# Kernel tuning notes

Measured on AMD Instinct MI355X. Metric: run time of the kernel, lower is better.

Reference implementation:

```python
import jax, jax.numpy as jnp
import numpy as np

H = 1024      # hidden_size
V = 50257     # output_size (vocab)
L = 10        # max_length

def setup_inputs() -> dict:
    key = jax.random.key(0)
    ks = jax.random.split(key, 16)
    s = 0.02
    f = jnp.float32
    return {
        "input_idx": jax.random.randint(ks[0], (1,), 0, V),
        "hidden": jax.random.normal(ks[1], (1, 1, H), f),
        "encoder_output": jax.random.normal(ks[2], (1, H), f),      # unused by forward (as in source)
        "encoder_outputs": jax.random.normal(ks[3], (L, H), f),
        "emb": jax.random.normal(ks[4], (V, H), f) * s,
        "attn_W": jax.random.normal(ks[5], (L, 2 * H), f) * s,
        "attn_b": jnp.zeros((L,), f),
        "comb_W": jax.random.normal(ks[6], (H, 2 * H), f) * s,
        "comb_b": jnp.zeros((H,), f),
        "W_ih": jax.random.normal(ks[7], (3 * H, H), f) * s,
        "W_hh": jax.random.normal(ks[8], (3 * H, H), f) * s,
        "b_ih": jnp.zeros((3 * H,), f),
        "b_hh": jnp.zeros((3 * H,), f),
        "out_W": jax.random.normal(ks[9], (V, H), f) * s,
        "out_b": jnp.zeros((V,), f),
    }

def reference(input_idx, hidden, encoder_output, encoder_outputs,
              emb, attn_W, attn_b, comb_W, comb_b,
              W_ih, W_hh, b_ih, b_hh, out_W, out_b):
    # embedding lookup, dropout = identity (eval mode)
    embedded = emb[input_idx]                       # [1, H]
    h0 = hidden[0]                                  # [1, H]
    # additive attention over encoder outputs
    concat = jnp.concatenate([embedded, h0], axis=1)            # [1, 2H]
    attn_weights = jax.nn.softmax(concat @ attn_W.T + attn_b, axis=1)  # [1, L]
    attn_applied = attn_weights @ encoder_outputs               # [1, H]
    # combine + relu
    x = jnp.concatenate([embedded, attn_applied], axis=1) @ comb_W.T + comb_b  # [1, H]
    x = jax.nn.relu(x)
    # single GRU step (torch gate order: r, z, n)
    gi = x @ W_ih.T + b_ih                          # [1, 3H]
    gh = h0 @ W_hh.T + b_hh                         # [1, 3H]
    ir, iz, in_ = jnp.split(gi, 3, axis=1)
    hr, hz, hn = jnp.split(gh, 3, axis=1)
    r = jax.nn.sigmoid(ir + hr)
    z = jax.nn.sigmoid(iz + hz)
    n = jnp.tanh(in_ + r * hn)
    h_new = (1.0 - z) * n + z * h0                  # [1, H]
    # output projection + log-softmax
    output = jax.nn.log_softmax(h_new @ out_W.T + out_b, axis=1)  # [1, V]
    return output, h_new[None], attn_weights
```

## Files before the change

### kernel.cpp

```cpp
#include <hip/hip_runtime.h>
#include <hip/hip_bf16.h>
#include <math.h>

#define H 1024
#define V 50257
#define L 10

#define RPC 16
#define NCHUNK ((V + RPC - 1) / RPC)

#define WS_AW     0
#define WS_GH     16
#define WS_HALF1  3104
#define WS_M2T    4128
#define WS_HNEW   14368
#define WS_LOGITS 15392
#define WS_PAIRS  65664

__device__ __forceinline__ float wave_reduce(float a) {
    #pragma unroll
    for (int off = 32; off > 0; off >>= 1) a += __shfl_down(a, off);
    return a;
}

__device__ __forceinline__ void lse_merge(float& m, float& s, float pm, float ps) {
    if (pm == -INFINITY) return;
    if (m == -INFINITY)  { m = pm; s = ps; }
    else if (pm <= m)    { s += ps * expf(pm - m); }
    else                 { s = s * expf(m - pm) + ps; m = pm; }
}

__device__ __forceinline__ float dot4(float4 a, float4 x) {
    return a.x * x.x + a.y * x.y + a.z * x.z + a.w * x.w;
}

__global__ __launch_bounds__(256) void k_stage1(
    const int* __restrict__ idx, const float* __restrict__ hidden,
    const float* __restrict__ enc_outs, const float* __restrict__ emb,
    const float* __restrict__ attn_W, const float* __restrict__ attn_b,
    const float* __restrict__ W_hh, const float* __restrict__ b_hh,
    const float* __restrict__ comb_W,
    float* __restrict__ ws, float* __restrict__ aw_out)
{
    const int b = blockIdx.x, t = threadIdx.x;
    const int wave = t >> 6, lane = t & 63;
    const float* erow = emb + (size_t)idx[0] * H;

    if (b == 0) {
        __shared__ float s_w[16];
        const float4* e4 = (const float4*)erow;
        const float4* h4 = (const float4*)hidden;
        for (int l = wave; l < L; l += 4) {
            const float4* w4 = (const float4*)(attn_W + (size_t)l * 2 * H);
            float acc = 0.f;
            #pragma unroll
            for (int ii = 0; ii < 8; ++ii) {
                const int i = lane + 64 * ii;
                const float4 a = w4[i];
                const float4 x = (i < 256) ? e4[i] : h4[i - 256];
                acc += dot4(a, x);
            }
            acc = wave_reduce(acc);
            if (lane == 0) s_w[l] = acc + attn_b[l];
        }
        __syncthreads();
        if (t == 0) {
            float m = -1e30f;
            #pragma unroll
            for (int l = 0; l < L; ++l) m = fmaxf(m, s_w[l]);
            float s = 0.f;
            #pragma unroll
            for (int l = 0; l < L; ++l) { s_w[l] = expf(s_w[l] - m); s += s_w[l]; }
            const float inv = 1.f / s;
            #pragma unroll
            for (int l = 0; l < L; ++l) s_w[l] *= inv;
        }
        __syncthreads();
        if (t < L) { ws[WS_AW + t] = s_w[t]; aw_out[t] = s_w[t]; }
    } else if (b <= 192) {
        const int r0 = (b - 1) * 16 + wave * 4;
        const float4* v4 = (const float4*)hidden;
        float4 hx[4];
        #pragma unroll
        for (int j = 0; j < 4; ++j) hx[j] = v4[lane + 64 * j];
        float a0 = 0.f, a1 = 0.f, a2 = 0.f, a3 = 0.f;
        const float4* w0 = (const float4*)(W_hh + (size_t)(r0 + 0) * H);
        const float4* w1 = (const float4*)(W_hh + (size_t)(r0 + 1) * H);
        const float4* w2 = (const float4*)(W_hh + (size_t)(r0 + 2) * H);
        const float4* w3 = (const float4*)(W_hh + (size_t)(r0 + 3) * H);
        #pragma unroll
        for (int j = 0; j < 4; ++j) {
            const int i = lane + 64 * j;
            a0 += dot4(w0[i], hx[j]); a1 += dot4(w1[i], hx[j]);
            a2 += dot4(w2[i], hx[j]); a3 += dot4(w3[i], hx[j]);
        }
        a0 = wave_reduce(a0); a1 = wave_reduce(a1);
        a2 = wave_reduce(a2); a3 = wave_reduce(a3);
        if (lane == 0) {
            ws[WS_GH + r0 + 0] = a0 + b_hh[r0 + 0];
            ws[WS_GH + r0 + 1] = a1 + b_hh[r0 + 1];
            ws[WS_GH + r0 + 2] = a2 + b_hh[r0 + 2];
            ws[WS_GH + r0 + 3] = a3 + b_hh[r0 + 3];
        }
    } else if (b <= 256) {
        const int r0 = (b - 193) * 16 + wave * 4;
        const float4* e4 = (const float4*)erow;
        float4 ex[4];
        #pragma unroll
        for (int j = 0; j < 4; ++j) ex[j] = e4[lane + 64 * j];
        float a0 = 0.f, a1 = 0.f, a2 = 0.f, a3 = 0.f;
        const float4* w0 = (const float4*)(comb_W + (size_t)(r0 + 0) * 2 * H);
        const float4* w1 = (const float4*)(comb_W + (size_t)(r0 + 1) * 2 * H);
        const float4* w2 = (const float4*)(comb_W + (size_t)(r0 + 2) * 2 * H);
        const float4* w3 = (const float4*)(comb_W + (size_t)(r0 + 3) * 2 * H);
        #pragma unroll
        for (int j = 0; j < 4; ++j) {
            const int i = lane + 64 * j;
            a0 += dot4(w0[i], ex[j]); a1 += dot4(w1[i], ex[j]);
            a2 += dot4(w2[i], ex[j]); a3 += dot4(w3[i], ex[j]);
        }
        a0 = wave_reduce(a0); a1 = wave_reduce(a1);
        a2 = wave_reduce(a2); a3 = wave_reduce(a3);
        if (lane == 0) {
            ws[WS_HALF1 + r0 + 0] = a0; ws[WS_HALF1 + r0 + 1] = a1;
            ws[WS_HALF1 + r0 + 2] = a2; ws[WS_HALF1 + r0 + 3] = a3;
        }
    } else {
        const int r = (b - 257) * 4 + wave;
        const float4* w4 = (const float4*)(comb_W + (size_t)r * 2 * H + H);
        float acc[L];
        #pragma unroll
        for (int l = 0; l < L; ++l) acc[l] = 0.f;
        #pragma unroll
        for (int j = 0; j < 4; ++j) {
            const int i = lane + 64 * j;
            const float4 w = w4[i];
            #pragma unroll
            for (int l = 0; l < L; ++l) {
                const float4 e = ((const float4*)(enc_outs + l * H))[i];
                acc[l] += dot4(w, e);
            }
        }
        #pragma unroll
        for (int l = 0; l < L; ++l) {
            const float r_ = wave_reduce(acc[l]);
            if (lane == 0) ws[WS_M2T + l * 1024 + r] = r_;
        }
    }
}

__global__ __launch_bounds__(256) void k_gi_gru(
    const float* __restrict__ W_ih, const float* __restrict__ b_ih,
    const float* __restrict__ comb_b, const float* __restrict__ hidden,
    float* __restrict__ ws, float* __restrict__ h_out)
{
    __shared__ float sx[1024];
    const int t = threadIdx.x;
    #pragma unroll
    for (int q = 0; q < 4; ++q) {
        const int e = t + q * 256;
        float acc = ws[WS_HALF1 + e] + comb_b[e];
        #pragma unroll
        for (int l = 0; l < L; ++l)
            acc += ws[WS_M2T + l * 1024 + e] * ws[WS_AW + l];
        sx[e] = fmaxf(acc, 0.f);
    }
    __syncthreads();
    const int wave = t >> 6, lane = t & 63;
    const int u = blockIdx.x * 4 + wave;
    const float4* x4 = (const float4*)sx;
    const float4* w0 = (const float4*)(W_ih + (size_t)u * H);
    const float4* w1 = (const float4*)(W_ih + (size_t)(H + u) * H);
    const float4* w2 = (const float4*)(W_ih + (size_t)(2 * H + u) * H);
    float a0 = 0.f, a1 = 0.f, a2 = 0.f;
    #pragma unroll
    for (int q = 0; q < 4; ++q) {
        const int i = lane + 64 * q;
        const float4 x = x4[i];
        a0 += dot4(w0[i], x);
        a1 += dot4(w1[i], x);
        a2 += dot4(w2[i], x);
    }
    a0 = wave_reduce(a0); a1 = wave_reduce(a1); a2 = wave_reduce(a2);
    if (lane == 0) {
        const float ir  = a0 + b_ih[u];
        const float iz  = a1 + b_ih[H + u];
        const float in_ = a2 + b_ih[2 * H + u];
        const float hr = ws[WS_GH + u];
        const float hz = ws[WS_GH + H + u];
        const float hn = ws[WS_GH + 2 * H + u];
        const float r = 1.f / (1.f + expf(-(ir + hr)));
        const float z = 1.f / (1.f + expf(-(iz + hz)));
        const float n = tanhf(in_ + r * hn);
        const float h = (1.f - z) * n + z * hidden[u];
        ws[WS_HNEW + u] = h;
        h_out[u] = h;
    }
}

__global__ __launch_bounds__(256) void k_out_mv(
    const float* __restrict__ out_W, const float* __restrict__ out_b,
    const float* __restrict__ ws_in, float* __restrict__ logits,
    float* __restrict__ pairs)
{
    __shared__ float sm[4], ss[4];
    const int wave = threadIdx.x >> 6, lane = threadIdx.x & 63;
    const int base = blockIdx.x * RPC + wave * 4;
    const float4* v4 = (const float4*)(ws_in + WS_HNEW);
    float4 hx[4];
    #pragma unroll
    for (int j = 0; j < 4; ++j) hx[j] = v4[lane + 64 * j];
    float wm = -INFINITY, wsum = 0.f;
    #pragma unroll
    for (int k = 0; k < 4; ++k) {
        const int row = base + k;
        if (row < V) {
            const float4* w4 = (const float4*)(out_W + (size_t)row * H);
            float acc = 0.f;
            #pragma unroll
            for (int j = 0; j < 4; ++j) acc += dot4(w4[lane + 64 * j], hx[j]);
            acc = wave_reduce(acc);
            if (lane == 0) {
                const float val = acc + out_b[row];
                logits[row] = val;
                lse_merge(wm, wsum, val, 1.f);
            }
        }
    }
    if (lane == 0) { sm[wave] = wm; ss[wave] = wsum; }
    __syncthreads();
    if (threadIdx.x == 0) {
        float m = -INFINITY, s = 0.f;
        #pragma unroll
        for (int w = 0; w < 4; ++w) lse_merge(m, s, sm[w], ss[w]);
        pairs[2 * blockIdx.x] = m; pairs[2 * blockIdx.x + 1] = s;
    }
}

__global__ __launch_bounds__(256) void k_write(
    const float* __restrict__ logits, const float* __restrict__ pairs,
    float* __restrict__ out)
{
    __shared__ float sm[256], ss[256];
    const int t = threadIdx.x;
    float m = -INFINITY, s = 0.f;
    for (int i = t; i < NCHUNK; i += 256) lse_merge(m, s, pairs[2 * i], pairs[2 * i + 1]);
    sm[t] = m; ss[t] = s; __syncthreads();
    for (int k = 128; k > 0; k >>= 1) {
        if (t < k) {
            float mm = sm[t], ssv = ss[t];
            lse_merge(mm, ssv, sm[t + k], ss[t + k]);
            sm[t] = mm; ss[t] = ssv;
        }
        __syncthreads();
    }
    const float M = sm[0], LS = logf(ss[0]);
    const int i = blockIdx.x * 256 + t;
    if (i < V) out[i] = logits[i] - M - LS;
}

extern "C" void kernel_launch(void* const* d_in, const int* in_sizes, int n_in,
                              void* d_out, int out_size, void* d_ws, size_t ws_size,
                              hipStream_t stream) {
    const int*   idx      = (const int*)  d_in[0];
    const float* hidden   = (const float*)d_in[1];
    const float* enc_outs = (const float*)d_in[3];
    const float* emb      = (const float*)d_in[4];
    const float* attn_W   = (const float*)d_in[5];
    const float* attn_b   = (const float*)d_in[6];
    const float* comb_W   = (const float*)d_in[7];
    const float* comb_b   = (const float*)d_in[8];
    const float* W_ih     = (const float*)d_in[9];
    const float* W_hh     = (const float*)d_in[10];
    const float* b_ih     = (const float*)d_in[11];
    const float* b_hh     = (const float*)d_in[12];
    const float* out_W    = (const float*)d_in[13];
    const float* out_b    = (const float*)d_in[14];

    float* ws  = (float*)d_ws;
    float* out = (float*)d_out;

    k_stage1<<<513, 256, 0, stream>>>(idx, hidden, enc_outs, emb,
                                      attn_W, attn_b, W_hh, b_hh, comb_W,
                                      ws, out + V + H);
    k_gi_gru<<<256, 256, 0, stream>>>(W_ih, b_ih, comb_b, hidden, ws, out + V);
    k_out_mv<<<NCHUNK, 256, 0, stream>>>(out_W, out_b, ws,
                                         ws + WS_LOGITS, ws + WS_PAIRS);
    k_write<<<(V + 255) / 256, 256, 0, stream>>>(ws + WS_LOGITS, ws + WS_PAIRS, out);
}
```

Measured before the change: 58.83 us.

## Fuse output matvec and log-softmax write into persistent kernel with grid barrier

Replaces the output projection kernel and the separate normalization kernel with one persistent kernel of 512 blocks. The blocks take row chunks from an atomic work counter, then meet at a software grid barrier (atomic counter plus spin) before each block reduces the per-chunk max/sum pairs and writes its slice of log-probabilities. This removes one kernel launch and the boundary between the two kernels. In exchange it adds an atomic per chunk and a spin barrier that assumes all 512 blocks are resident at the same time. If they are not, the barrier deadlocks.

```diff
diff --git a/kernel.cpp b/kernel.cpp
--- a/kernel.cpp
+++ b/kernel.cpp
@@ -8,6 +8,7 @@
 
 #define RPC 16
 #define NCHUNK ((V + RPC - 1) / RPC)
+#define NBLK3 512
 
 #define WS_AW     0
 #define WS_GH     16
@@ -16,6 +17,7 @@
 #define WS_HNEW   14368
 #define WS_LOGITS 15392
 #define WS_PAIRS  65664
+#define WS_CNT    72000
 
 __device__ __forceinline__ float wave_reduce(float a) {
     #pragma unroll
@@ -47,6 +49,10 @@
     const float* erow = emb + (size_t)idx[0] * H;
 
     if (b == 0) {
+        if (t == 0) {
+            ((int*)(ws + WS_CNT))[0] = NBLK3;
+            ((int*)(ws + WS_CNT))[1] = 0;
+        }
         __shared__ float s_w[16];
         const float4* e4 = (const float4*)erow;
         const float4* h4 = (const float4*)hidden;
@@ -198,65 +204,85 @@
     }
 }
 
-__global__ __launch_bounds__(256) void k_out_mv(
+__global__ __launch_bounds__(256) void k_out_full(
     const float* __restrict__ out_W, const float* __restrict__ out_b,
-    const float* __restrict__ ws_in, float* __restrict__ logits,
-    float* __restrict__ pairs)
+    float* __restrict__ ws, float* __restrict__ out)
 {
     __shared__ float sm[4], ss[4];
-    const int wave = threadIdx.x >> 6, lane = threadIdx.x & 63;
-    const int base = blockIdx.x * RPC + wave * 4;
-    const float4* v4 = (const float4*)(ws_in + WS_HNEW);
+    __shared__ float rm[256], rs[256];
+    __shared__ int s_c;
+    const int b = blockIdx.x, t = threadIdx.x;
+    const int wave = t >> 6, lane = t & 63;
+    int* cnt = (int*)(ws + WS_CNT);
+    float* logits = ws + WS_LOGITS;
+    float* pairs  = ws + WS_PAIRS;
+
+    const float4* v4 = (const float4*)(ws + WS_HNEW);
     float4 hx[4];
     #pragma unroll
     for (int j = 0; j < 4; ++j) hx[j] = v4[lane + 64 * j];
-    float wm = -INFINITY, wsum = 0.f;
-    #pragma unroll
-    for (int k = 0; k < 4; ++k) {
-        const int row = base + k;
-        if (row < V) {
-            const float4* w4 = (const float4*)(out_W + (size_t)row * H);
-            float acc = 0.f;
-            #pragma unroll
-            for (int j = 0; j < 4; ++j) acc += dot4(w4[lane + 64 * j], hx[j]);
-            acc = wave_reduce(acc);
-            if (lane == 0) {
-                const float val = acc + out_b[row];
-                logits[row] = val;
-                lse_merge(wm, wsum, val, 1.f);
+
+    int c = b;
+    while (c < NCHUNK) {
+        const int base = c * RPC + wave * 4;
+        float wm = -INFINITY, wsum = 0.f;
+        #pragma unroll
+        for (int k = 0; k < 4; ++k) {
+            const int row = base + k;
+            if (row < V) {
+                const float4* w4 = (const float4*)(out_W + (size_t)row * H);
+                float acc = 0.f;
+                #pragma unroll
+                for (int j = 0; j < 4; ++j) acc += dot4(w4[lane + 64 * j], hx[j]);
+                acc = wave_reduce(acc);
+                if (lane == 0) {
+                    const float val = acc + out_b[row];
+                    logits[row] = val;
+                    lse_merge(wm, wsum, val, 1.f);
+                }
             }
         }
-    }
-    if (lane == 0) { sm[wave] = wm; ss[wave] = wsum; }
+        if (lane == 0) { sm[wave] = wm; ss[wave] = wsum; }
+        if (t == 0) s_c = atomicAdd(&cnt[0], 1);
+        __syncthreads();
+        if (t == 0) {
+            float m = -INFINITY, s = 0.f;
+            #pragma unroll
+            for (int w = 0; w < 4; ++w) lse_merge(m, s, sm[w], ss[w]);
+            pairs[2 * c] = m; pairs[2 * c + 1] = s;
+        }
+        const int cn = s_c;
+        __syncthreads();
+        c = cn;
+    }
+
+    __threadfence();
     __syncthreads();
-    if (threadIdx.x == 0) {
+    if (t == 0) {
+        atomicAdd(&cnt[1], 1);
+        while (atomicAdd(&cnt[1], 0) < NBLK3) __builtin_amdgcn_s_sleep(2);
+    }
+    __syncthreads();
+    __threadfence();
+
+    if (b * 256 < V) {
         float m = -INFINITY, s = 0.f;
-        #pragma unroll
-        for (int w = 0; w < 4; ++w) lse_merge(m, s, sm[w], ss[w]);
-        pairs[2 * blockIdx.x] = m; pairs[2 * blockIdx.x + 1] = s;
-    }
-}
-
-__global__ __launch_bounds__(256) void k_write(
-    const float* __restrict__ logits, const float* __restrict__ pairs,
-    float* __restrict__ out)
-{
-    __shared__ float sm[256], ss[256];
-    const int t = threadIdx.x;
-    float m = -INFINITY, s = 0.f;
-    for (int i = t; i < NCHUNK; i += 256) lse_merge(m, s, pairs[2 * i], pairs[2 * i + 1]);
-    sm[t] = m; ss[t] = s; __syncthreads();
-    for (int k = 128; k > 0; k >>= 1) {
-        if (t < k) {
-            float mm = sm[t], ssv = ss[t];
-            lse_merge(mm, ssv, sm[t + k], ss[t + k]);
-            sm[t] = mm; ss[t] = ssv;
-        }
-        __syncthreads();
-    }
-    const float M = sm[0], LS = logf(ss[0]);
-    const int i = blockIdx.x * 256 + t;
-    if (i < V) out[i] = logits[i] - M - LS;
+        for (int i = t; i < NCHUNK; i += 256)
+            lse_merge(m, s, pairs[2 * i], pairs[2 * i + 1]);
+        rm[t] = m; rs[t] = s;
+        __syncthreads();
+        for (int k = 128; k > 0; k >>= 1) {
+            if (t < k) {
+                float mm = rm[t], ssv = rs[t];
+                lse_merge(mm, ssv, rm[t + k], rs[t + k]);
+                rm[t] = mm; rs[t] = ssv;
+            }
+            __syncthreads();
+        }
+        const float M = rm[0], LS = logf(rs[0]);
+        const int i = b * 256 + t;
+        if (i < V) out[i] = logits[i] - M - LS;
+    }
 }
 
 extern "C" void kernel_launch(void* const* d_in, const int* in_sizes, int n_in,
@@ -284,7 +310,5 @@
                                       attn_W, attn_b, W_hh, b_hh, comb_W,
                                       ws, out + V + H);
     k_gi_gru<<<256, 256, 0, stream>>>(W_ih, b_ih, comb_b, hidden, ws, out + V);
-    k_out_mv<<<NCHUNK, 256, 0, stream>>>(out_W, out_b, ws,
-                                         ws + WS_LOGITS, ws + WS_PAIRS);
-    k_write<<<(V + 255) / 256, 256, 0, stream>>>(ws + WS_LOGITS, ws + WS_PAIRS, out);
-}
+    k_out_full<<<NBLK3, 256, 0, stream>>>(out_W, out_b, ws, out);
+}
```

After: 195.9 us. 233% more time.
